# Performance work log

Hardware: AMD Instinct MI355X
Metric: run time of the kernel (lower is better)

The kernel has to match this reference:

```python
import jax, jax.numpy as jnp
import numpy as np

DIM = 1024
HEADS = 16
DIM_HEAD = 64
INNER = HEADS * DIM_HEAD  # 1024
EPS = 1e-5


def setup_inputs() -> dict:
    key = jax.random.key(0)
    ks = jax.random.split(key, 5)
    x = jax.random.normal(ks[0], (4, 2048, DIM), dtype=jnp.float32)
    ln_gamma = jnp.ones((DIM,), dtype=jnp.float32)
    ln_beta = jnp.zeros((DIM,), dtype=jnp.float32)
    # nn.Linear weights ~ U(-1/sqrt(fan_in), 1/sqrt(fan_in)); stored as (out, in) in torch,
    # here kept as (in, out) for x @ W.
    lim = 1.0 / np.sqrt(DIM)
    w_qkv = jax.random.uniform(ks[1], (DIM, 3 * INNER), minval=-lim, maxval=lim, dtype=jnp.float32)
    lim2 = 1.0 / np.sqrt(INNER)
    w_out = jax.random.uniform(ks[2], (INNER, DIM), minval=-lim2, maxval=lim2, dtype=jnp.float32)
    return {"x": x, "ln_gamma": ln_gamma, "ln_beta": ln_beta, "w_qkv": w_qkv, "w_out": w_out}


def reference(x, ln_gamma, ln_beta, w_qkv, w_out):
    b, n, d = x.shape
    # LayerNorm
    mu = jnp.mean(x, axis=-1, keepdims=True)
    var = jnp.mean(jnp.square(x - mu), axis=-1, keepdims=True)
    xn = (x - mu) * jax.lax.rsqrt(var + EPS) * ln_gamma + ln_beta
    # QKV projection
    qkv = xn @ w_qkv  # (b, n, 3*inner)
    q, k, v = jnp.split(qkv, 3, axis=-1)
    def to_heads(t):
        return t.reshape(b, n, HEADS, DIM_HEAD).transpose(0, 2, 1, 3)  # (b,h,n,dh)
    q, k, v = to_heads(q), to_heads(k), to_heads(v)
    scale = DIM_HEAD ** -0.5
    scores = jnp.einsum('bhqd,bhkd->bhqk', q, k) * scale
    causal = jnp.tril(jnp.ones((n, n), dtype=bool))
    scores = jnp.where(causal, scores, -jnp.inf)
    probs = jax.nn.softmax(scores, axis=-1)
    out = jnp.einsum('bhqk,bhkd->bhqd', probs, v)
    out = out.transpose(0, 2, 1, 3).reshape(b, n, INNER)
    return out @ w_out
```

## Files before the change

kernel.cpp:

```cpp
#include <hip/hip_runtime.h>
#include <hip/hip_bf16.h>

#define DIM 1024
#define HEADS 16
#define DH 64
#define SEQ 2048
#define BATCH 4
#define ROWS (BATCH * SEQ)
#define NQKV (3 * DIM)

typedef __attribute__((ext_vector_type(8))) __bf16 bf16x8;
typedef __attribute__((ext_vector_type(4))) __bf16 bf16x4;
typedef __attribute__((ext_vector_type(4))) float f32x4;

__device__ inline void gload16(const void* g, void* l) {
  __builtin_amdgcn_global_load_lds(
      (const __attribute__((address_space(1))) void*)g,
      (__attribute__((address_space(3))) void*)l, 16, 0, 0);
}

__device__ inline float fast_exp2(float x) {
#if __has_builtin(__builtin_amdgcn_exp2f)
  return __builtin_amdgcn_exp2f(x);
#else
  return exp2f(x);
#endif
}

__global__ __launch_bounds__(256) void ln_kernel(
    const float* __restrict__ x, const float* __restrict__ gamma,
    const float* __restrict__ beta, __bf16* __restrict__ xnb) {
  const int row = blockIdx.x;
  const int tid = threadIdx.x;
  const float4* xr = (const float4*)(x + (size_t)row * DIM);
  float4 v = xr[tid];
  float s1 = v.x + v.y + v.z + v.w;
  float s2 = v.x * v.x + v.y * v.y + v.z * v.z + v.w * v.w;
#pragma unroll
  for (int d = 32; d > 0; d >>= 1) {
    s1 += __shfl_xor(s1, d);
    s2 += __shfl_xor(s2, d);
  }
  __shared__ float red1[4], red2[4];
  const int wave = tid >> 6, lane = tid & 63;
  if (lane == 0) { red1[wave] = s1; red2[wave] = s2; }
  __syncthreads();
  s1 = red1[0] + red1[1] + red1[2] + red1[3];
  s2 = red2[0] + red2[1] + red2[2] + red2[3];
  const float mean = s1 * (1.0f / DIM);
  const float var = s2 * (1.0f / DIM) - mean * mean;
  const float rstd = rsqrtf(var + 1e-5f);
  float4 g = ((const float4*)gamma)[tid];
  float4 b = ((const float4*)beta)[tid];
  bf16x4 o;
  o[0] = (__bf16)((v.x - mean) * rstd * g.x + b.x);
  o[1] = (__bf16)((v.y - mean) * rstd * g.y + b.y);
  o[2] = (__bf16)((v.z - mean) * rstd * g.z + b.z);
  o[3] = (__bf16)((v.w - mean) * rstd * g.w + b.w);
  *(bf16x4*)(xnb + (size_t)row * DIM + tid * 4) = o;
}

__global__ __launch_bounds__(256) void transpose_cast(
    const float* __restrict__ in, __bf16* __restrict__ outT, int rows, int cols) {
  __shared__ float tile[32][33];
  const int tx = threadIdx.x & 31, ty = threadIdx.x >> 5;
  const int c0 = blockIdx.x * 32, r0 = blockIdx.y * 32;
#pragma unroll
  for (int rr = ty; rr < 32; rr += 8)
    tile[rr][tx] = in[(size_t)(r0 + rr) * cols + c0 + tx];
  __syncthreads();
#pragma unroll
  for (int rr = ty; rr < 32; rr += 8)
    outT[(size_t)(c0 + rr) * rows + r0 + tx] = (__bf16)tile[tx][rr];
}

template <int MODE>
__global__ __launch_bounds__(256) void gemm128(
    const __bf16* __restrict__ A, const __bf16* __restrict__ Bt, int K, int N,
    float* __restrict__ Cout, __bf16* __restrict__ qb, __bf16* __restrict__ kb,
    __bf16* __restrict__ vtb) {
  __shared__ __bf16 As[2][128 * 32];
  __shared__ __bf16 Bs[2][128 * 32];
  const int tid = threadIdx.x;
  const int wave = tid >> 6, lane = tid & 63;
  const int quad = lane >> 4, l16 = lane & 15;
  const int wm = wave >> 1, wn = wave & 1;
  const size_t tileM = (size_t)blockIdx.x * 128;
  const size_t tileN = (size_t)blockIdx.y * 128;
  const int sel = (MODE == 1) ? (int)(tileN >> 10) : 0;
  const bool vmode = (MODE == 1) && (sel == 2);

  f32x4 acc[4][4];
#pragma unroll
  for (int i = 0; i < 4; ++i)
#pragma unroll
    for (int j = 0; j < 4; ++j) acc[i][j] = (f32x4){0.f, 0.f, 0.f, 0.f};

  const int sr = lane >> 2;
  const int sc = lane & 3;
  const int ck = (l16 >> 1) & 3;

  const __bf16* Abase = A + tileM * (size_t)K;
  const __bf16* Bbase = Bt + tileN * (size_t)K;

  auto stage = [&](int buf, int k0) {
#pragma unroll
    for (int p = 0; p < 2; ++p) {
      const int rbase = p * 64 + wave * 16;
      const int row = rbase + sr;
      const int gc = (sc ^ ((row >> 1) & 3)) << 3;
      gload16(Abase + (size_t)row * K + k0 + gc, &As[buf][rbase * 32]);
      gload16(Bbase + (size_t)row * K + k0 + gc, &Bs[buf][rbase * 32]);
    }
  };

  const int NIT = K >> 5;
  stage(0, 0);
  for (int it = 0; it < NIT; ++it) {
    __syncthreads();
    if (it + 1 < NIT) stage((it + 1) & 1, (it + 1) << 5);
    const int buf = it & 1;
    bf16x8 af[4], bfr[4];
#pragma unroll
    for (int mt = 0; mt < 4; ++mt)
      af[mt] =
          *(const bf16x8*)&As[buf][(wm * 64 + mt * 16 + l16) * 32 + ((quad ^ ck) << 3)];
#pragma unroll
    for (int nt = 0; nt < 4; ++nt)
      bfr[nt] =
          *(const bf16x8*)&Bs[buf][(wn * 64 + nt * 16 + l16) * 32 + ((quad ^ ck) << 3)];
    if (vmode) {
#pragma unroll
      for (int mt = 0; mt < 4; ++mt)
#pragma unroll
        for (int nt = 0; nt < 4; ++nt)
          acc[mt][nt] = __builtin_amdgcn_mfma_f32_16x16x32_bf16(af[mt], bfr[nt],
                                                                acc[mt][nt], 0, 0, 0);
    } else {
#pragma unroll
      for (int mt = 0; mt < 4; ++mt)
#pragma unroll
        for (int nt = 0; nt < 4; ++nt)
          acc[mt][nt] = __builtin_amdgcn_mfma_f32_16x16x32_bf16(bfr[nt], af[mt],
                                                                acc[mt][nt], 0, 0, 0);
    }
  }

  if (MODE == 0) {
#pragma unroll
    for (int mt = 0; mt < 4; ++mt) {
      const size_t m = tileM + wm * 64 + mt * 16 + l16;
#pragma unroll
      for (int nt = 0; nt < 4; ++nt) {
        const size_t n0 = tileN + wn * 64 + nt * 16 + quad * 4;
        *(f32x4*)&Cout[m * (size_t)N + n0] = acc[mt][nt];
      }
    }
  } else if (sel < 2) {
    __bf16* dst = (sel == 0) ? qb : kb;
#pragma unroll
    for (int mt = 0; mt < 4; ++mt) {
      const size_t m = tileM + wm * 64 + mt * 16 + l16;
      const int b = (int)(m >> 11), seq = (int)(m & 2047);
#pragma unroll
      for (int nt = 0; nt < 4; ++nt) {
        const int c = (int)(tileN & 1023) + wn * 64 + nt * 16 + quad * 4;
        const int head = c >> 6, dh = c & 63;
        bf16x4 pk;
#pragma unroll
        for (int r = 0; r < 4; ++r) pk[r] = (__bf16)acc[mt][nt][r];
        *(bf16x4*)&dst[(((size_t)b * HEADS + head) * SEQ + seq) * DH + dh] = pk;
      }
    }
  } else {
#pragma unroll
    for (int nt = 0; nt < 4; ++nt) {
      const int c = (int)(tileN & 1023) + wn * 64 + nt * 16 + l16;
      const int head = c >> 6, dh = c & 63;
#pragma unroll
      for (int mt = 0; mt < 4; ++mt) {
        const size_t m0 = tileM + wm * 64 + mt * 16 + quad * 4;
        const int b = (int)(m0 >> 11), seq = (int)(m0 & 2047);
        bf16x4 pk;
#pragma unroll
        for (int r = 0; r < 4; ++r) pk[r] = (__bf16)acc[mt][nt][r];
        *(bf16x4*)&vtb[(((size_t)b * HEADS + head) * DH + dh) * SEQ + seq] = pk;
      }
    }
  }
}

__global__ __launch_bounds__(256, 4) void attn_kernel(
    const __bf16* __restrict__ qb, const __bf16* __restrict__ kb,
    const __bf16* __restrict__ vtb, __bf16* __restrict__ ob) {
  const int bh = blockIdx.x;
  const int by = blockIdx.y;
  const int tid = threadIdx.x;
  const int wave = tid >> 6, lane = tid & 63;
  const int quad = lane >> 4, l16 = lane & 15;

  __shared__ __bf16 Ks[2][64 * 64];
  __shared__ __bf16 Vs[2][64 * 64];
  __shared__ __bf16 Ps[4][16 * 36];

  const __bf16* kg = kb + (size_t)bh * SEQ * DH;
  const __bf16* vg = vtb + (size_t)bh * DH * SEQ;

  const int i1 = by, i2 = 31 - by;
  const int T = 33;

  const int kr = lane >> 3, kc = lane & 7;

  auto stage = [&](int buf, int j) {
#pragma unroll
    for (int p = 0; p < 2; ++p) {
      const int rbase = wave * 16 + p * 8;
      const int row = rbase + kr;
      gload16(kg + (size_t)(j * 64 + row) * DH + ((kc ^ (row & 7)) << 3),
              &Ks[buf][rbase * 64]);
      gload16(vg + (size_t)row * SEQ + j * 64 + ((kc ^ (row & 7)) << 3),
              &Vs[buf][rbase * 64]);
    }
  };

  const float QSCALE = 0.125f * 1.44269504088896f;
  bf16x8 qf[2];
  auto load_q = [&](int i) {
    const __bf16* qbase = qb + ((size_t)bh * SEQ + (size_t)i * 64 + wave * 16) * DH;
#pragma unroll
    for (int ks = 0; ks < 2; ++ks) {
      bf16x8 v = *(const bf16x8*)(qbase + l16 * DH + ks * 32 + quad * 8);
#pragma unroll
      for (int e = 0; e < 8; ++e) v[e] = (__bf16)((float)v[e] * QSCALE);
      qf[ks] = v;
    }
  };

  float m_i, l_i;
  f32x4 o_acc[4];
  auto reset_state = [&]() {
    m_i = -1e30f;
    l_i = 0.f;
#pragma unroll
    for (int md = 0; md < 4; ++md) o_acc[md] = (f32x4){0.f, 0.f, 0.f, 0.f};
  };
  const int b_out = bh >> 4, h_out = bh & 15;
  auto epilogue = [&](int i) {
    float lsum = l_i;
    lsum += __shfl_xor(lsum, 16);
    lsum += __shfl_xor(lsum, 32);
    const float inv = __builtin_amdgcn_rcpf(lsum);
    const int seq = i * 64 + wave * 16 + l16;
    __bf16* dst = ob + ((size_t)b_out * SEQ + seq) * DIM + h_out * DH;
#pragma unroll
    for (int md = 0; md < 4; ++md) {
      bf16x4 pk;
#pragma unroll
      for (int r = 0; r < 4; ++r) pk[r] = (__bf16)(o_acc[md][r] * inv);
      *(bf16x4*)(dst + md * 16 + quad * 4) = pk;
    }
  };

  load_q(i1);
  reset_state();
  stage(0, 0);

  for (int t = 0; t < T; ++t) {
    __syncthreads();
    if (t + 1 < T) {
      const int jn = (t + 1 <= by) ? (t + 1) : (t - by);
      stage((t + 1) & 1, jn);
    }
    const int buf = t & 1;
    const int i = (t <= by) ? i1 : i2;
    const int j = (t <= by) ? t : (t - by - 1);
    const bool diag = (j == i);

    f32x4 sa[4];
#pragma unroll
    for (int nt = 0; nt < 4; ++nt) sa[nt] = (f32x4){0.f, 0.f, 0.f, 0.f};
#pragma unroll
    for (int nt = 0; nt < 4; ++nt)
#pragma unroll
      for (int ks = 0; ks < 2; ++ks) {
        bf16x8 kf = *(const bf16x8*)&Ks[buf][(nt * 16 + l16) * 64 +
                                            (((ks * 4 + quad) ^ (l16 & 7)) << 3)];
        sa[nt] = __builtin_amdgcn_mfma_f32_16x16x32_bf16(kf, qf[ks], sa[nt], 0, 0, 0);
      }

    if (diag) {
      const int qrl = wave * 16 + l16;
#pragma unroll
      for (int nt = 0; nt < 4; ++nt)
#pragma unroll
        for (int r = 0; r < 4; ++r) {
          const int kvl = nt * 16 + quad * 4 + r;
          if (kvl > qrl) sa[nt][r] = -1e30f;
        }
    }

    {
      float mx = -1e30f;
#pragma unroll
      for (int nt = 0; nt < 4; ++nt) {
        const float a0 = fmaxf(fmaxf(sa[nt][0], sa[nt][1]), sa[nt][2]);
        mx = fmaxf(mx, fmaxf(a0, sa[nt][3]));
      }
      mx = fmaxf(mx, __shfl_xor(mx, 16));
      mx = fmaxf(mx, __shfl_xor(mx, 32));
      if (__all(mx - m_i <= 8.f)) {
        float rs = 0.f;
#pragma unroll
        for (int nt = 0; nt < 4; ++nt)
#pragma unroll
          for (int r = 0; r < 4; ++r) {
            const float p = fast_exp2(sa[nt][r] - m_i);
            sa[nt][r] = p;
            rs += p;
          }
        l_i += rs;
      } else {
        const float mnew = fmaxf(m_i, mx);
        const float alpha = fast_exp2(m_i - mnew);
        m_i = mnew;
        float rs = 0.f;
#pragma unroll
        for (int nt = 0; nt < 4; ++nt)
#pragma unroll
          for (int r = 0; r < 4; ++r) {
            const float p = fast_exp2(sa[nt][r] - mnew);
            sa[nt][r] = p;
            rs += p;
          }
        l_i = l_i * alpha + rs;
#pragma unroll
        for (int md = 0; md < 4; ++md)
#pragma unroll
          for (int r = 0; r < 4; ++r) o_acc[md][r] *= alpha;
      }
    }

#pragma unroll
    for (int c = 0; c < 2; ++c) {
#pragma unroll
      for (int ntl = 0; ntl < 2; ++ntl) {
        const int nt = c * 2 + ntl;
        bf16x4 pk;
#pragma unroll
        for (int r = 0; r < 4; ++r) pk[r] = (__bf16)sa[nt][r];
        *(bf16x4*)&Ps[wave][l16 * 36 + ntl * 16 + quad * 4] = pk;
      }
      bf16x8 pf = *(const bf16x8*)&Ps[wave][l16 * 36 + quad * 8];
#pragma unroll
      for (int md = 0; md < 4; ++md) {
        bf16x8 vf = *(const bf16x8*)&Vs[buf][(md * 16 + l16) * 64 +
                                            (((c * 4 + quad) ^ (l16 & 7)) << 3)];
        o_acc[md] = __builtin_amdgcn_mfma_f32_16x16x32_bf16(vf, pf, o_acc[md], 0, 0, 0);
      }
    }

    if (t == by) {
      epilogue(i1);
      reset_state();
      load_q(i2);
    }
  }
  epilogue(i2);
}

extern "C" void kernel_launch(void* const* d_in, const int* in_sizes, int n_in,
                              void* d_out, int out_size, void* d_ws, size_t ws_size,
                              hipStream_t stream) {
  const float* x = (const float*)d_in[0];
  const float* gamma = (const float*)d_in[1];
  const float* beta = (const float*)d_in[2];
  const float* w_qkv = (const float*)d_in[3];
  const float* w_out = (const float*)d_in[4];
  float* out = (float*)d_out;

  char* ws = (char*)d_ws;
  const size_t MB = 1024 * 1024;
  __bf16* xnb = (__bf16*)ws;
  __bf16* wqkvT = (__bf16*)(ws + 16 * MB);
  __bf16* woutT = (__bf16*)(ws + 24 * MB);
  __bf16* qbuf = (__bf16*)(ws + 32 * MB);
  __bf16* kbuf = (__bf16*)(ws + 48 * MB);
  __bf16* vtbuf = (__bf16*)(ws + 64 * MB);
  __bf16* attnb = xnb;

  ln_kernel<<<ROWS, 256, 0, stream>>>(x, gamma, beta, xnb);
  transpose_cast<<<dim3(NQKV / 32, DIM / 32), 256, 0, stream>>>(w_qkv, wqkvT, DIM, NQKV);
  transpose_cast<<<dim3(DIM / 32, DIM / 32), 256, 0, stream>>>(w_out, woutT, DIM, DIM);
  gemm128<1><<<dim3(ROWS / 128, NQKV / 128), 256, 0, stream>>>(
      xnb, wqkvT, DIM, NQKV, nullptr, qbuf, kbuf, vtbuf);
  attn_kernel<<<dim3(BATCH * HEADS, 16), 256, 0, stream>>>(qbuf, kbuf, vtbuf, attnb);
  gemm128<0><<<dim3(ROWS / 128, DIM / 128), 256, 0, stream>>>(
      attnb, woutT, DIM, DIM, out, nullptr, nullptr, nullptr);
}
```

Baseline: 288.8 us.

## Rewrite GEMMs as 256x128 8-wave ping-pong pipelined kernels with XCD-aware tile mapping

Replaces the 128x128, 4-wave bf16 GEMM with a 256x128 tile, 512-thread kernel. It uses a K-step of 64, splits the A tile into halves that are staged separately, and places explicit vmcnt waits and barriers so global-to-LDS loads overlap with MFMA clusters, raising priority with s_setprio around the MFMAs. The block index is remapped so consecutive tiles land on the same XCD for L2 reuse, and the LDS swizzle is changed to suit the wider K rows. This targets the latency and sync overhead of the old double-buffered loop. In exchange it relies on hand-counted vmcnt values and leaves one block per CU, which could stall or become fragile.

```diff
diff --git a/kernel.cpp b/kernel.cpp
--- a/kernel.cpp
+++ b/kernel.cpp
@@ -75,96 +75,172 @@
 }
 
 template <int MODE>
-__global__ __launch_bounds__(256) void gemm128(
-    const __bf16* __restrict__ A, const __bf16* __restrict__ Bt, int K, int N,
-    float* __restrict__ Cout, __bf16* __restrict__ qb, __bf16* __restrict__ kb,
-    __bf16* __restrict__ vtb) {
-  __shared__ __bf16 As[2][128 * 32];
-  __shared__ __bf16 Bs[2][128 * 32];
+__global__ __launch_bounds__(512, 1) void gemmP(
+    const __bf16* __restrict__ A, const __bf16* __restrict__ Bt, const int K,
+    const int N, float* __restrict__ Cout, __bf16* __restrict__ qb,
+    __bf16* __restrict__ kb, __bf16* __restrict__ vtb) {
+  __shared__ __bf16 As[2][2][128 * 64];
+  __shared__ __bf16 Bs[2][128 * 64];
   const int tid = threadIdx.x;
   const int wave = tid >> 6, lane = tid & 63;
   const int quad = lane >> 4, l16 = lane & 15;
-  const int wm = wave >> 1, wn = wave & 1;
-  const size_t tileM = (size_t)blockIdx.x * 128;
-  const size_t tileN = (size_t)blockIdx.y * 128;
+  const int wm = wave >> 2, wn = wave & 3;
+
+  const int nwg = (int)gridDim.x;
+  const int cpx = nwg >> 3;
+  const int wg = ((int)blockIdx.x & 7) * cpx + ((int)blockIdx.x >> 3);
+  const size_t tileM = (size_t)(wg & 31) * 256;
+  const size_t tileN = (size_t)(wg >> 5) * 128;
   const int sel = (MODE == 1) ? (int)(tileN >> 10) : 0;
   const bool vmode = (MODE == 1) && (sel == 2);
 
-  f32x4 acc[4][4];
-#pragma unroll
-  for (int i = 0; i < 4; ++i)
-#pragma unroll
-    for (int j = 0; j < 4; ++j) acc[i][j] = (f32x4){0.f, 0.f, 0.f, 0.f};
-
-  const int sr = lane >> 2;
-  const int sc = lane & 3;
-  const int ck = (l16 >> 1) & 3;
+  f32x4 acc[8][2];
+#pragma unroll
+  for (int i = 0; i < 8; ++i)
+#pragma unroll
+    for (int j = 0; j < 2; ++j) acc[i][j] = (f32x4){0.f, 0.f, 0.f, 0.f};
 
   const __bf16* Abase = A + tileM * (size_t)K;
   const __bf16* Bbase = Bt + tileN * (size_t)K;
 
-  auto stage = [&](int buf, int k0) {
+  const int slr = tid >> 3, sc = tid & 7;
+  const int scol = (sc ^ (slr & 7)) << 3;
+
+  auto stageA = [&](int buf, int h, int kt) {
+    const size_t col = (size_t)(kt << 6) + scol;
 #pragma unroll
     for (int p = 0; p < 2; ++p) {
-      const int rbase = p * 64 + wave * 16;
-      const int row = rbase + sr;
-      const int gc = (sc ^ ((row >> 1) & 3)) << 3;
-      gload16(Abase + (size_t)row * K + k0 + gc, &As[buf][rbase * 32]);
-      gload16(Bbase + (size_t)row * K + k0 + gc, &Bs[buf][rbase * 32]);
-    }
-  };
-
-  const int NIT = K >> 5;
-  stage(0, 0);
-  for (int it = 0; it < NIT; ++it) {
-    __syncthreads();
-    if (it + 1 < NIT) stage((it + 1) & 1, (it + 1) << 5);
-    const int buf = it & 1;
-    bf16x8 af[4], bfr[4];
-#pragma unroll
-    for (int mt = 0; mt < 4; ++mt)
-      af[mt] =
-          *(const bf16x8*)&As[buf][(wm * 64 + mt * 16 + l16) * 32 + ((quad ^ ck) << 3)];
-#pragma unroll
-    for (int nt = 0; nt < 4; ++nt)
-      bfr[nt] =
-          *(const bf16x8*)&Bs[buf][(wn * 64 + nt * 16 + l16) * 32 + ((quad ^ ck) << 3)];
+      const int gr = p * 128 + h * 64 + slr;
+      const int lr = p * 64 + slr;
+      gload16(Abase + (size_t)gr * K + col, &As[buf][h][lr * 64 + sc * 8]);
+    }
+  };
+  auto stageB = [&](int buf, int kt) {
+    const size_t col = (size_t)(kt << 6) + scol;
+#pragma unroll
+    for (int p = 0; p < 2; ++p) {
+      const int lr = p * 64 + slr;
+      gload16(Bbase + (size_t)lr * K + col, &Bs[buf][lr * 64 + sc * 8]);
+    }
+  };
+
+  const int rpc = quad ^ (l16 & 7);
+  auto ldA = [&](int buf, int mt, int ks) -> bf16x8 {
+    const int lr = wm * 64 + (mt & 3) * 16 + l16;
+    return *(const bf16x8*)&As[buf][mt >> 2][lr * 64 + ((rpc ^ (ks << 2)) << 3)];
+  };
+  auto ldB = [&](int buf, int nt, int ks) -> bf16x8 {
+    const int lr = wn * 32 + nt * 16 + l16;
+    return *(const bf16x8*)&Bs[buf][lr * 64 + ((rpc ^ (ks << 2)) << 3)];
+  };
+
+  auto cluster = [&](const bf16x8* af, bf16x8 bf0, bf16x8 bf1, int mb) {
+    __builtin_amdgcn_s_setprio(1);
     if (vmode) {
 #pragma unroll
-      for (int mt = 0; mt < 4; ++mt)
-#pragma unroll
-        for (int nt = 0; nt < 4; ++nt)
-          acc[mt][nt] = __builtin_amdgcn_mfma_f32_16x16x32_bf16(af[mt], bfr[nt],
-                                                                acc[mt][nt], 0, 0, 0);
+      for (int mt = 0; mt < 4; ++mt) {
+        acc[mb + mt][0] = __builtin_amdgcn_mfma_f32_16x16x32_bf16(
+            af[mt], bf0, acc[mb + mt][0], 0, 0, 0);
+        acc[mb + mt][1] = __builtin_amdgcn_mfma_f32_16x16x32_bf16(
+            af[mt], bf1, acc[mb + mt][1], 0, 0, 0);
+      }
     } else {
 #pragma unroll
-      for (int mt = 0; mt < 4; ++mt)
-#pragma unroll
-        for (int nt = 0; nt < 4; ++nt)
-          acc[mt][nt] = __builtin_amdgcn_mfma_f32_16x16x32_bf16(bfr[nt], af[mt],
-                                                                acc[mt][nt], 0, 0, 0);
-    }
+      for (int mt = 0; mt < 4; ++mt) {
+        acc[mb + mt][0] = __builtin_amdgcn_mfma_f32_16x16x32_bf16(
+            bf0, af[mt], acc[mb + mt][0], 0, 0, 0);
+        acc[mb + mt][1] = __builtin_amdgcn_mfma_f32_16x16x32_bf16(
+            bf1, af[mt], acc[mb + mt][1], 0, 0, 0);
+      }
+    }
+    __builtin_amdgcn_s_setprio(0);
+  };
+
+  stageA(0, 0, 0);
+  stageB(0, 0);
+  stageA(0, 1, 0);
+
+  const int NT = K >> 6;
+  bf16x8 af[4], b00, b01, b10, b11;
+
+  for (int t = 0; t < NT - 1; ++t) {
+    const int buf = t & 1, nbuf = buf ^ 1, kn = t + 1;
+    stageA(nbuf, 0, kn);
+    asm volatile("s_waitcnt vmcnt(4)" ::: "memory");
+    __builtin_amdgcn_s_barrier();
+    asm volatile("" ::: "memory");
+    __builtin_amdgcn_sched_barrier(0);
+#pragma unroll
+    for (int mt = 0; mt < 4; ++mt) af[mt] = ldA(buf, mt, 0);
+    b00 = ldB(buf, 0, 0);
+    b01 = ldB(buf, 1, 0);
+    cluster(af, b00, b01, 0);
+    stageB(nbuf, kn);
+#pragma unroll
+    for (int mt = 0; mt < 4; ++mt) af[mt] = ldA(buf, mt, 1);
+    b10 = ldB(buf, 0, 1);
+    b11 = ldB(buf, 1, 1);
+    cluster(af, b10, b11, 0);
+    stageA(nbuf, 1, kn);
+    asm volatile("s_waitcnt vmcnt(6)" ::: "memory");
+    __builtin_amdgcn_s_barrier();
+    asm volatile("" ::: "memory");
+    __builtin_amdgcn_sched_barrier(0);
+#pragma unroll
+    for (int mt = 0; mt < 4; ++mt) af[mt] = ldA(buf, 4 + mt, 0);
+    cluster(af, b00, b01, 4);
+#pragma unroll
+    for (int mt = 0; mt < 4; ++mt) af[mt] = ldA(buf, 4 + mt, 1);
+    cluster(af, b10, b11, 4);
   }
 
+  {
+    const int buf = (NT - 1) & 1;
+    asm volatile("s_waitcnt vmcnt(2)" ::: "memory");
+    __builtin_amdgcn_s_barrier();
+    asm volatile("" ::: "memory");
+    __builtin_amdgcn_sched_barrier(0);
+#pragma unroll
+    for (int mt = 0; mt < 4; ++mt) af[mt] = ldA(buf, mt, 0);
+    b00 = ldB(buf, 0, 0);
+    b01 = ldB(buf, 1, 0);
+    cluster(af, b00, b01, 0);
+#pragma unroll
+    for (int mt = 0; mt < 4; ++mt) af[mt] = ldA(buf, mt, 1);
+    b10 = ldB(buf, 0, 1);
+    b11 = ldB(buf, 1, 1);
+    cluster(af, b10, b11, 0);
+    asm volatile("s_waitcnt vmcnt(0)" ::: "memory");
+    __builtin_amdgcn_s_barrier();
+    asm volatile("" ::: "memory");
+    __builtin_amdgcn_sched_barrier(0);
+#pragma unroll
+    for (int mt = 0; mt < 4; ++mt) af[mt] = ldA(buf, 4 + mt, 0);
+    cluster(af, b00, b01, 4);
+#pragma unroll
+    for (int mt = 0; mt < 4; ++mt) af[mt] = ldA(buf, 4 + mt, 1);
+    cluster(af, b10, b11, 4);
+  }
+
   if (MODE == 0) {
 #pragma unroll
-    for (int mt = 0; mt < 4; ++mt) {
-      const size_t m = tileM + wm * 64 + mt * 16 + l16;
-#pragma unroll
-      for (int nt = 0; nt < 4; ++nt) {
-        const size_t n0 = tileN + wn * 64 + nt * 16 + quad * 4;
+    for (int mt = 0; mt < 8; ++mt) {
+      const size_t m = tileM + wm * 128 + mt * 16 + l16;
+#pragma unroll
+      for (int nt = 0; nt < 2; ++nt) {
+        const size_t n0 = tileN + wn * 32 + nt * 16 + quad * 4;
         *(f32x4*)&Cout[m * (size_t)N + n0] = acc[mt][nt];
       }
     }
   } else if (sel < 2) {
     __bf16* dst = (sel == 0) ? qb : kb;
 #pragma unroll
-    for (int mt = 0; mt < 4; ++mt) {
-      const size_t m = tileM + wm * 64 + mt * 16 + l16;
+    for (int mt = 0; mt < 8; ++mt) {
+      const size_t m = tileM + wm * 128 + mt * 16 + l16;
       const int b = (int)(m >> 11), seq = (int)(m & 2047);
 #pragma unroll
-      for (int nt = 0; nt < 4; ++nt) {
-        const int c = (int)(tileN & 1023) + wn * 64 + nt * 16 + quad * 4;
+      for (int nt = 0; nt < 2; ++nt) {
+        const int c = (int)(tileN & 1023) + wn * 32 + nt * 16 + quad * 4;
         const int head = c >> 6, dh = c & 63;
         bf16x4 pk;
 #pragma unroll
@@ -174,12 +250,12 @@
     }
   } else {
 #pragma unroll
-    for (int nt = 0; nt < 4; ++nt) {
-      const int c = (int)(tileN & 1023) + wn * 64 + nt * 16 + l16;
+    for (int nt = 0; nt < 2; ++nt) {
+      const int c = (int)(tileN & 1023) + wn * 32 + nt * 16 + l16;
       const int head = c >> 6, dh = c & 63;
 #pragma unroll
-      for (int mt = 0; mt < 4; ++mt) {
-        const size_t m0 = tileM + wm * 64 + mt * 16 + quad * 4;
+      for (int mt = 0; mt < 8; ++mt) {
+        const size_t m0 = tileM + wm * 128 + mt * 16 + quad * 4;
         const int b = (int)(m0 >> 11), seq = (int)(m0 & 2047);
         bf16x4 pk;
 #pragma unroll
@@ -391,9 +467,9 @@
   ln_kernel<<<ROWS, 256, 0, stream>>>(x, gamma, beta, xnb);
   transpose_cast<<<dim3(NQKV / 32, DIM / 32), 256, 0, stream>>>(w_qkv, wqkvT, DIM, NQKV);
   transpose_cast<<<dim3(DIM / 32, DIM / 32), 256, 0, stream>>>(w_out, woutT, DIM, DIM);
-  gemm128<1><<<dim3(ROWS / 128, NQKV / 128), 256, 0, stream>>>(
+  gemmP<1><<<dim3((ROWS / 256) * (NQKV / 128)), 512, 0, stream>>>(
       xnb, wqkvT, DIM, NQKV, nullptr, qbuf, kbuf, vtbuf);
   attn_kernel<<<dim3(BATCH * HEADS, 16), 256, 0, stream>>>(qbuf, kbuf, vtbuf, attnb);
-  gemm128<0><<<dim3(ROWS / 128, DIM / 128), 256, 0, stream>>>(
+  gemmP<0><<<dim3((ROWS / 256) * (DIM / 128)), 512, 0, stream>>>(
       attnb, woutT, DIM, DIM, out, nullptr, nullptr, nullptr);
 }
```

New measurement: 285.5 us. Within noise of the previous version (-1.1%).
